# Kernel tuning notes

Measured on AMD Instinct MI355X. Metric: run time of the kernel, lower is better.

The kernel has to match this reference:

```python
import jax, jax.numpy as jnp
import numpy as np

B, G, N, D = 2, 2, 2048, 512
H, DH = 8, 64
DI = H * DH  # dim_inner = 512


def rmsnorm(x, gamma):
    # x: [b, g, n, d]; original normalizes over feature dim (F.normalize, eps=1e-12)
    norm = jnp.linalg.norm(x, axis=-1, keepdims=True)
    normed = x / jnp.maximum(norm, 1e-12)
    return normed * jnp.sqrt(jnp.asarray(x.shape[-1], x.dtype)) * gamma[None, :, None, :]


def setup_inputs() -> dict:
    key = jax.random.key(0)
    ks = jax.random.split(key, 8)
    x = jax.random.normal(ks[0], (B, G, N, D), dtype=jnp.float32)
    mask = jax.random.randint(ks[1], (B, N), 0, 2) > 0
    gamma_q = jnp.ones((G, D), dtype=jnp.float32)
    gamma_c = jnp.ones((G, D), dtype=jnp.float32)
    s = 0.02
    wq = jax.random.normal(ks[2], (G, DI, D), dtype=jnp.float32) * s
    wkv = jax.random.normal(ks[3], (G, 2 * DI, D), dtype=jnp.float32) * s
    wout = jax.random.normal(ks[4], (G, D, DI), dtype=jnp.float32) * s
    null_kv = jax.random.normal(ks[5], (2, G, H, 1, DH), dtype=jnp.float32)
    return {"x": x, "mask": mask, "gamma_q": gamma_q, "gamma_c": gamma_c,
            "wq": wq, "wkv": wkv, "wout": wout, "null_kv": null_kv}


def reference(x, mask, gamma_q, gamma_c, wq, wkv, wout, null_kv):
    b, g, n, d = x.shape
    # prenorm (context = x, so both norms applied to same input)
    xq = rmsnorm(x, gamma_q)
    xc = rmsnorm(x, gamma_c)
    # grouped 1x1 conv projections == per-group matmuls
    q = jnp.einsum('bgnd,ged->bgne', xq, wq)                 # [b,g,n,DI]
    kv = jnp.einsum('bgnd,ged->bgne', xc, wkv)               # [b,g,n,2*DI]
    k, v = jnp.split(kv, 2, axis=-1)
    def split_heads(t):
        return t.reshape(b, g, n, H, DH).transpose(0, 1, 3, 2, 4)  # [b,g,h,n,dh]
    q, k, v = map(split_heads, (q, k, v))
    # null kv: concat along sequence dim
    nk = jnp.broadcast_to(null_kv[0][None], (b, g, H, 1, DH))
    nv = jnp.broadcast_to(null_kv[1][None], (b, g, H, 1, DH))
    k = jnp.concatenate([nk, k], axis=-2)                    # [b,g,h,n+1,dh]
    v = jnp.concatenate([nv, v], axis=-2)
    # attention
    scale = DH ** -0.5
    scores = jnp.einsum('bghid,bghjd->bghij', q, k) * scale  # [b,g,h,n,n+1]
    m = jnp.concatenate([jnp.ones((b, 1), dtype=bool), mask], axis=-1)  # pad True for null kv
    scores = jnp.where(m[:, None, None, None, :], scores, jnp.asarray(-1e30, scores.dtype))
    attn = jax.nn.softmax(scores, axis=-1)
    out = jnp.einsum('bghij,bghjd->bghid', attn, v)          # [b,g,h,n,dh]
    out = out.transpose(0, 1, 3, 2, 4).reshape(b, g, n, DI)  # merge heads
    out = jnp.einsum('bgne,gde->bgnd', out, wout)
    return out
```

## Files before the change

### kernel.cpp

```cpp
#include <hip/hip_runtime.h>
#include <stdint.h>

typedef unsigned short u16;
typedef __attribute__((ext_vector_type(8))) short  bf16x8;
typedef __attribute__((ext_vector_type(8))) u16    u16x8;
typedef __attribute__((ext_vector_type(4))) u16    u16x4;
typedef __attribute__((ext_vector_type(4))) float  f32x4;
typedef __attribute__((ext_vector_type(2))) unsigned u32x2;

#define SEQ 2048
#define DIM 512
#define NH  8
#define NBG 4
#define QSCALE 0.18033688011112042f

__device__ __forceinline__ float bf2f(u16 u) { return __uint_as_float(((unsigned)u) << 16); }
__device__ __forceinline__ u16 f2bf(float f) {
  unsigned u = __float_as_uint(f);
  return (u16)((u + 0x7FFFu + ((u >> 16) & 1u)) >> 16);
}
__device__ __forceinline__ float h2f(u16 u) { return (float)__builtin_bit_cast(_Float16, u); }
__device__ __forceinline__ u16 f2h(float f) { return __builtin_bit_cast(unsigned short, (_Float16)f); }

__device__ __forceinline__ float ex2(float x) {
#if __has_builtin(__builtin_amdgcn_exp2f)
  return __builtin_amdgcn_exp2f(x);
#else
  return exp2f(x);
#endif
}

__device__ __forceinline__ void gload_lds16(const void* g, void* l) {
#if __has_builtin(__builtin_amdgcn_global_load_lds)
  __builtin_amdgcn_global_load_lds((__attribute__((address_space(1))) void*)g,
                                   (__attribute__((address_space(3))) void*)l, 16, 0, 0);
#else
  *(u16x8*)l = *(const u16x8*)g;
#endif
}

__device__ __forceinline__ int float_mode(const void* gq) {
  unsigned w0 = *(const unsigned*)gq;
  return (w0 == 0x3F800000u) ? 1 : ((w0 == 0x3C003C00u) ? 2 : 0);
}
__device__ __forceinline__ int mask_mode(const void* maskp) {
  const unsigned* mw = (const unsigned*)maskp;
  bool all01 = true, lowhit = false, f32ish = true;
#pragma unroll
  for (int i = 0; i < 64; i++) {
    unsigned v = mw[i];
    all01 = all01 && (v <= 1u);
    lowhit = lowhit || ((v & 0xFFFFu) == 0x3F80u) || ((v & 0xFFFFu) == 0x3C00u);
    f32ish = f32ish && (v == 0u || v == 0x3F800000u);
  }
  return all01 ? 0 : (lowhit ? 1 : (f32ish ? 2 : 3));
}
__device__ __forceinline__ bool mask_at(const void* m, int idx, int mode) {
  if (mode == 0) return ((const int*)m)[idx] != 0;
  if (mode == 1) return ((const u16*)m)[idx] != 0;
  if (mode == 2) return ((const float*)m)[idx] != 0.f;
  return ((const unsigned char*)m)[idx] != 0;
}
__device__ __forceinline__ float ldf(const void* p, int i, int mode) {
  if (mode == 1) return ((const float*)p)[i];
  if (mode == 2) return h2f(((const u16*)p)[i]);
  return bf2f(((const u16*)p)[i]);
}

__global__ __launch_bounds__(256) void pre_kernel(
    const void* __restrict__ x, const void* __restrict__ gq, const void* __restrict__ gc,
    const void* __restrict__ wq, const void* __restrict__ wkv, const void* __restrict__ wout,
    const void* __restrict__ nkv, const void* __restrict__ maskp,
    u16* __restrict__ wqb, u16* __restrict__ wkvb, u16* __restrict__ woutb, u16* __restrict__ nkvb,
    u16* __restrict__ xn, int* __restrict__ gidx, int* __restrict__ nv)
{
  const int NWQ = 2*512*512, NWKV = 2*1024*512, NWOUT = 2*512*512;
  if (blockIdx.x >= 3073) {
    __shared__ int sc[2][256];
    __shared__ int tot;
    int b = blockIdx.x - 3073;
    int t = threadIdx.x;
    const int smode = mask_mode(maskp);
    int base = t * 8;
    int loc[8]; int c = 0;
#pragma unroll
    for (int i = 0; i < 8; i++) { loc[i] = mask_at(maskp, b * SEQ + base + i, smode) ? 1 : 0; c += loc[i]; }
    sc[0][t] = c;
    int src = 0, v = c;
    for (int off = 1; off < 256; off <<= 1) {
      __syncthreads();
      int add = (t >= off) ? sc[src][t - off] : 0;
      v += add;
      sc[src ^ 1][t] = v;
      src ^= 1;
    }
    int run = v - c;
#pragma unroll
    for (int i = 0; i < 8; i++) { if (loc[i]) gidx[b * SEQ + run] = base + i; run += loc[i]; }
    if (t == 255) { nv[b] = v; tot = v; }
    __syncthreads();
#pragma unroll
    for (int i = 0; i < 8; i++) {
      int p = base + i;
      if (p >= tot) gidx[b * SEQ + p] = 0;
    }
    return;
  }
  int mode = float_mode(gq);
  if (blockIdx.x < 1025) {
    int loc = (blockIdx.x * 256 + threadIdx.x) * 8;
    const void* s; u16* d; int fold = 0; const void* gam = nullptr; int gbase = 0; float ex = 1.f;
    if (loc < NWQ) { s = wq; d = wqb; fold = 1; gam = gq; gbase = ((loc >> 18) << 9) | (loc & 511); ex = QSCALE; }
    else { loc -= NWQ;
      if (loc < NWKV) { s = wkv; d = wkvb; fold = 1; gam = gc; gbase = ((loc >> 19) << 9) | (loc & 511); }
      else { loc -= NWKV;
        if (loc < NWOUT) { s = wout; d = woutb; }
        else { loc -= NWOUT; if (loc < 2048) { s = nkv; d = nkvb; } else return; } } }
    u16x8 o;
#pragma unroll
    for (int j = 0; j < 8; j++) {
      float v = ldf(s, loc + j, mode) * ex;
      if (fold) v *= ldf(gam, gbase + j, mode);
      o[j] = f2bf(v);
    }
    *(u16x8*)(d + loc) = o;
    return;
  }
  int row  = (blockIdx.x - 1025) * 4 + (threadIdx.x >> 6);
  int lane = threadIdx.x & 63;
  float f[8];
  if (mode == 1) {
    const float* xr = (const float*)x + (size_t)row * DIM + lane * 8;
    f32x4 a = *(const f32x4*)xr, b2 = *(const f32x4*)(xr + 4);
#pragma unroll
    for (int i = 0; i < 4; i++) { f[i] = a[i]; f[i + 4] = b2[i]; }
  } else if (mode == 2) {
    u16x8 v = *(const u16x8*)((const u16*)x + (size_t)row * DIM + lane * 8);
#pragma unroll
    for (int i = 0; i < 8; i++) f[i] = h2f(v[i]);
  } else {
    u16x8 v = *(const u16x8*)((const u16*)x + (size_t)row * DIM + lane * 8);
#pragma unroll
    for (int i = 0; i < 8; i++) f[i] = bf2f(v[i]);
  }
  float ss = 0.f;
#pragma unroll
  for (int i = 0; i < 8; i++) ss += f[i] * f[i];
#pragma unroll
  for (int off = 32; off; off >>= 1) ss += __shfl_xor(ss, off);
  float scale = 22.62741699796952f / fmaxf(sqrtf(ss), 1e-12f);
  u16x8 o;
#pragma unroll
  for (int i = 0; i < 8; i++) o[i] = f2bf(f[i] * scale);
  *(u16x8*)(xn + (size_t)row * DIM + lane * 8) = o;
}

__global__ __launch_bounds__(256, 4) void gemm_qkv(
    const u16* __restrict__ A, const u16* __restrict__ wqb, const u16* __restrict__ wkvb,
    u16* __restrict__ qb, u16* __restrict__ kb, u16* __restrict__ vtb,
    const int* __restrict__ gidx, const int* __restrict__ nv)
{
  __shared__ u16 As[128 * 64], Bs[64 * 64];
  int bg = blockIdx.z, g = bg & 1;
  int y = blockIdx.y;
  const u16* Bw; int Ncols, bn0, isq;
  if (y < 8) { Bw = wqb;  Ncols = 512;  bn0 = y * 64;       isq = 1; }
  else       { Bw = wkvb; Ncols = 1024; bn0 = (y - 8) * 64; isq = 0; }
  const int M = SEQ, K = DIM, ldc = 512;
  int bm0 = blockIdx.x * 128;
  if (!isq) {
    int nvb = nv[bg >> 1];
    if (bm0 >= ((nvb + 127) & ~127)) return;
  }
  int tid = threadIdx.x, w = tid >> 6, l = tid & 63;
  int li = l & 15, lg = l >> 4;
  int wr = w >> 1, wc = w & 1;
  const u16* Ab = A + (size_t)bg * M * K;
  const u16* Bb = Bw + (size_t)g * Ncols * K;
  int arow[4];
#pragma unroll
  for (int i = 0; i < 4; i++) {
    int r = bm0 + ((i * 256 + tid) >> 3);
    arow[i] = isq ? r : gidx[(bg >> 1) * SEQ + r];
  }
  f32x4 acc[4][2];
#pragma unroll
  for (int m = 0; m < 4; m++)
#pragma unroll
    for (int n = 0; n < 2; n++) acc[m][n] = (f32x4){0.f, 0.f, 0.f, 0.f};
  for (int kt = 0; kt < K; kt += 64) {
#pragma unroll
    for (int i = 0; i < 4; i++) {
      int ch = i * 256 + tid;
      gload_lds16(Ab + (size_t)arow[i] * K + kt + ((ch & 7) << 3), &As[ch * 8]);
    }
#pragma unroll
    for (int i = 0; i < 2; i++) {
      int ch = i * 256 + tid;
      gload_lds16(Bb + (size_t)(bn0 + (ch >> 3)) * K + kt + ((ch & 7) << 3), &Bs[ch * 8]);
    }
    __syncthreads();
#pragma unroll
    for (int kk = 0; kk < 2; kk++) {
      bf16x8 a[4], b[2];
#pragma unroll
      for (int m = 0; m < 4; m++) a[m] = *(const bf16x8*)&As[(wr * 64 + m * 16 + li) * 64 + kk * 32 + lg * 8];
#pragma unroll
      for (int n = 0; n < 2; n++) b[n] = *(const bf16x8*)&Bs[(wc * 32 + n * 16 + li) * 64 + kk * 32 + lg * 8];
      __builtin_amdgcn_s_setprio(1);
#pragma unroll
      for (int m = 0; m < 4; m++)
#pragma unroll
        for (int n = 0; n < 2; n++)
          acc[m][n] = __builtin_amdgcn_mfma_f32_16x16x32_bf16(a[m], b[n], acc[m][n], 0, 0, 0);
      __builtin_amdgcn_s_setprio(0);
    }
    __syncthreads();
  }
  if (isq) {
#pragma unroll
    for (int m = 0; m < 4; m++) {
#pragma unroll
      for (int n = 0; n < 2; n++) {
        int row = bm0 + wr * 64 + m * 16 + lg * 4;
        int col = bn0 + wc * 32 + n * 16 + li;
        u16* cp = qb + (size_t)bg * M * ldc + (size_t)row * ldc + col;
#pragma unroll
        for (int r = 0; r < 4; r++) cp[(size_t)r * ldc] = f2bf(acc[m][n][r]);
      }
    }
  } else {
#pragma unroll
    for (int m = 0; m < 4; m++) {
#pragma unroll
      for (int n = 0; n < 2; n++) {
        int row = bm0 + wr * 64 + m * 16 + lg * 4;
        int col = bn0 + wc * 32 + n * 16 + li;
        if (col < 512) {
          u16* cp = kb + (size_t)bg * M * ldc + (size_t)row * ldc + col;
#pragma unroll
          for (int r = 0; r < 4; r++) cp[(size_t)r * ldc] = f2bf(acc[m][n][r]);
        } else {
          u16x4 pk;
#pragma unroll
          for (int r = 0; r < 4; r++) pk[r] = f2bf(acc[m][n][r]);
          *(u16x4*)&vtb[(size_t)bg * 512 * M + (size_t)(col - 512) * M + row] = pk;
        }
      }
    }
  }
}

__global__ __launch_bounds__(256, 4) void gemm_out(
    const u16* __restrict__ A, const u16* __restrict__ Bw,
    void* __restrict__ Cout, const void* __restrict__ gq0)
{
  __shared__ u16 As[128 * 64], Bs[64 * 64];
  const int M = SEQ, K = DIM, ldc = 512;
  int bg = blockIdx.z, g = bg & 1;
  int bm0 = blockIdx.x * 128, bn0 = blockIdx.y * 64;
  int tid = threadIdx.x, w = tid >> 6, l = tid & 63;
  int li = l & 15, lg = l >> 4;
  int wr = w >> 1, wc = w & 1;
  const u16* Ab = A + (size_t)bg * M * K;
  const u16* Bb = Bw + (size_t)g * 512 * K;
  f32x4 acc[4][2];
#pragma unroll
  for (int m = 0; m < 4; m++)
#pragma unroll
    for (int n = 0; n < 2; n++) acc[m][n] = (f32x4){0.f, 0.f, 0.f, 0.f};
  for (int kt = 0; kt < K; kt += 64) {
#pragma unroll
    for (int i = 0; i < 4; i++) {
      int ch = i * 256 + tid;
      gload_lds16(Ab + (size_t)(bm0 + (ch >> 3)) * K + kt + ((ch & 7) << 3), &As[ch * 8]);
    }
#pragma unroll
    for (int i = 0; i < 2; i++) {
      int ch = i * 256 + tid;
      gload_lds16(Bb + (size_t)(bn0 + (ch >> 3)) * K + kt + ((ch & 7) << 3), &Bs[ch * 8]);
    }
    __syncthreads();
#pragma unroll
    for (int kk = 0; kk < 2; kk++) {
      bf16x8 a[4], b[2];
#pragma unroll
      for (int m = 0; m < 4; m++) a[m] = *(const bf16x8*)&As[(wr * 64 + m * 16 + li) * 64 + kk * 32 + lg * 8];
#pragma unroll
      for (int n = 0; n < 2; n++) b[n] = *(const bf16x8*)&Bs[(wc * 32 + n * 16 + li) * 64 + kk * 32 + lg * 8];
      __builtin_amdgcn_s_setprio(1);
#pragma unroll
      for (int m = 0; m < 4; m++)
#pragma unroll
        for (int n = 0; n < 2; n++)
          acc[m][n] = __builtin_amdgcn_mfma_f32_16x16x32_bf16(a[m], b[n], acc[m][n], 0, 0, 0);
      __builtin_amdgcn_s_setprio(0);
    }
    __syncthreads();
  }
  int mode = float_mode(gq0);
#pragma unroll
  for (int m = 0; m < 4; m++) {
#pragma unroll
    for (int n = 0; n < 2; n++) {
      int row = bm0 + wr * 64 + m * 16 + lg * 4;
      int col = bn0 + wc * 32 + n * 16 + li;
      if (mode == 1) {
        float* cp = (float*)Cout + (size_t)bg * M * ldc + (size_t)row * ldc + col;
#pragma unroll
        for (int r = 0; r < 4; r++) cp[(size_t)r * ldc] = acc[m][n][r];
      } else if (mode == 2) {
        u16* cp = (u16*)Cout + (size_t)bg * M * ldc + (size_t)row * ldc + col;
#pragma unroll
        for (int r = 0; r < 4; r++) cp[(size_t)r * ldc] = f2h(acc[m][n][r]);
      } else {
        u16* cp = (u16*)Cout + (size_t)bg * M * ldc + (size_t)row * ldc + col;
#pragma unroll
        for (int r = 0; r < 4; r++) cp[(size_t)r * ldc] = f2bf(acc[m][n][r]);
      }
    }
  }
}

__global__ __launch_bounds__(256, 2) void attn_kernel(
    const u16* __restrict__ q, const u16* __restrict__ k, const u16* __restrict__ vt,
    const u16* __restrict__ nkv, const int* __restrict__ nv, u16* __restrict__ ao)
{
  __shared__ __align__(16) u16 Kb[2][64 * 64];
  __shared__ __align__(16) u16 Vb[2][64 * 64];
  __shared__ __align__(16) u16 Ps[4][16 * 72];
  const int bid = blockIdx.x;
  const int h = bid & 7, bg = (bid >> 3) & 3, ib = bid >> 5;
  const int g = bg & 1;
  const int tid = threadIdx.x, w = tid >> 6, l = tid & 63;
  const int li = l & 15, lg = l >> 4;
  const int i0 = ib * 128 + w * 32;
  const int nvb = nv[bg >> 1];
  const int NT = (nvb + 63) >> 6;

  auto stage = [&](int t, int buf) {
    int jb = t * 64;
#pragma unroll
    for (int p = 0; p < 2; p++) {
      int idx = p * 256 + tid;
      int r = idx >> 3, G = idx & 7;
      int c = (G ^ (r & 7)) << 3;
      gload_lds16(k + ((size_t)bg * SEQ + jb + r) * DIM + h * 64 + c, &Kb[buf][idx * 8]);
    }
#pragma unroll
    for (int p = 0; p < 2; p++) {
      int idx = p * 256 + tid;
      int r = idx >> 3, G = idx & 7;
      int c = (G ^ (r & 7)) << 3;
      gload_lds16(vt + ((size_t)bg * DIM + h * 64 + r) * SEQ + jb + c, &Vb[buf][idx * 8]);
    }
  };

  if (NT > 0) stage(0, 0);

  bf16x8 qf[2][2];
#pragma unroll
  for (int rg = 0; rg < 2; rg++)
#pragma unroll
    for (int kk = 0; kk < 2; kk++)
      qf[rg][kk] = *(const bf16x8*)&q[((size_t)bg * SEQ + i0 + rg * 16 + li) * DIM + h * 64 + kk * 32 + lg * 8];

  bf16x8 ones;
#pragma unroll
  for (int r = 0; r < 8; r++) ones[r] = (short)0x3F80;

  const u16* nk = nkv + ((size_t)g * NH + h) * 64;
  const u16* nvp = nkv + ((size_t)(2 + g) * NH + h) * 64;
  f32x4 oacc[2][4], lacc[2];
#pragma unroll
  for (int rg = 0; rg < 2; rg++) {
    float s = 0.f;
#pragma unroll
    for (int kk = 0; kk < 2; kk++)
#pragma unroll
      for (int r = 0; r < 8; r++)
        s += bf2f((u16)qf[rg][kk][r]) * bf2f(nk[kk * 32 + lg * 8 + r]);
    s += __shfl_xor(s, 16); s += __shfl_xor(s, 32);
    float pn = ex2(s);
    lacc[rg] = (f32x4){pn, pn, pn, pn};
#pragma unroll
    for (int dm = 0; dm < 4; dm++) {
      f32x4 o;
#pragma unroll
      for (int r = 0; r < 4; r++) o[r] = pn * bf2f(nvp[dm * 16 + lg * 4 + r]);
      oacc[rg][dm] = o;
    }
  }
  __syncthreads();

  for (int t = 0; t < NT; t++) {
    int cur = t & 1;
    if (t + 1 < NT) stage(t + 1, cur ^ 1);
    const bool tail = (t == NT - 1);

    bf16x8 kf[4][2];
#pragma unroll
    for (int jm = 0; jm < 4; jm++)
#pragma unroll
      for (int kk = 0; kk < 2; kk++) {
        int gsw = ((kk * 4 + lg) ^ (li & 7)) << 3;
        kf[jm][kk] = *(const bf16x8*)&Kb[cur][(jm * 16 + li) * 64 + gsw];
      }

    f32x4 s4[2][4];
    __builtin_amdgcn_s_setprio(1);
#pragma unroll
    for (int rg = 0; rg < 2; rg++)
#pragma unroll
      for (int jm = 0; jm < 4; jm++) {
        f32x4 z = {0.f, 0.f, 0.f, 0.f};
        z = __builtin_amdgcn_mfma_f32_16x16x32_bf16(kf[jm][0], qf[rg][0], z, 0, 0, 0);
        z = __builtin_amdgcn_mfma_f32_16x16x32_bf16(kf[jm][1], qf[rg][1], z, 0, 0, 0);
        s4[rg][jm] = z;
      }
    __builtin_amdgcn_s_setprio(0);

    int jb = t * 64;
#pragma unroll
    for (int rg = 0; rg < 2; rg++) {
      u16* pb = &Ps[w][0];
#pragma unroll
      for (int jm = 0; jm < 4; jm++) {
        unsigned u0 = __float_as_uint(ex2(s4[rg][jm][0]));
        unsigned u1 = __float_as_uint(ex2(s4[rg][jm][1]));
        unsigned u2 = __float_as_uint(ex2(s4[rg][jm][2]));
        unsigned u3 = __float_as_uint(ex2(s4[rg][jm][3]));
        unsigned w01 = __builtin_amdgcn_perm(u1, u0, 0x07060302u);
        unsigned w23 = __builtin_amdgcn_perm(u3, u2, 0x07060302u);
        if (tail) {
          int e0 = jb + jm * 16 + lg * 4;
          unsigned t01 = (e0 + 0 < nvb ? 0x0000FFFFu : 0u) | (e0 + 1 < nvb ? 0xFFFF0000u : 0u);
          unsigned t23 = (e0 + 2 < nvb ? 0x0000FFFFu : 0u) | (e0 + 3 < nvb ? 0xFFFF0000u : 0u);
          w01 &= t01; w23 &= t23;
        }
        *(u32x2*)&Ps[w][li * 72 + jm * 16 + lg * 4] = (u32x2){w01, w23};
      }
      bf16x8 pf0 = *(const bf16x8*)&pb[li * 72 + lg * 8];
      bf16x8 pf1 = *(const bf16x8*)&pb[li * 72 + 32 + lg * 8];
      __builtin_amdgcn_s_setprio(1);
      lacc[rg] = __builtin_amdgcn_mfma_f32_16x16x32_bf16(ones, pf0, lacc[rg], 0, 0, 0);
      lacc[rg] = __builtin_amdgcn_mfma_f32_16x16x32_bf16(ones, pf1, lacc[rg], 0, 0, 0);
#pragma unroll
      for (int dm = 0; dm < 4; dm++) {
        int gsw0 = ((0 * 4 + lg) ^ (li & 7)) << 3;
        int gsw1 = ((1 * 4 + lg) ^ (li & 7)) << 3;
        bf16x8 vf0 = *(const bf16x8*)&Vb[cur][(dm * 16 + li) * 64 + gsw0];
        bf16x8 vf1 = *(const bf16x8*)&Vb[cur][(dm * 16 + li) * 64 + gsw1];
        oacc[rg][dm] = __builtin_amdgcn_mfma_f32_16x16x32_bf16(vf0, pf0, oacc[rg][dm], 0, 0, 0);
        oacc[rg][dm] = __builtin_amdgcn_mfma_f32_16x16x32_bf16(vf1, pf1, oacc[rg][dm], 0, 0, 0);
      }
      __builtin_amdgcn_s_setprio(0);
    }
    __syncthreads();
  }

#pragma unroll
  for (int rg = 0; rg < 2; rg++) {
    float inv = 1.f / lacc[rg][0];
#pragma unroll
    for (int dm = 0; dm < 4; dm++) {
      u16x4 o;
#pragma unroll
      for (int r = 0; r < 4; r++) o[r] = f2bf(oacc[rg][dm][r] * inv);
      *(u16x4*)&ao[((size_t)bg * SEQ + i0 + rg * 16 + li) * DIM + h * 64 + dm * 16 + lg * 4] = o;
    }
  }
}

extern "C" void kernel_launch(void* const* d_in, const int* in_sizes, int n_in,
                              void* d_out, int out_size, void* d_ws, size_t ws_size,
                              hipStream_t stream) {
  const void* x    = d_in[0];
  const void* msk  = d_in[1];
  const void* gq   = d_in[2];
  const void* gc   = d_in[3];
  const void* wq   = d_in[4];
  const void* wkv  = d_in[5];
  const void* wout = d_in[6];
  const void* nkv  = d_in[7];

  u16* base = (u16*)d_ws;
  const size_t SLOT = (size_t)NBG * SEQ * DIM;
  u16* xn = base + 0 * SLOT;
  u16* ao = base + 0 * SLOT;
  u16* qb = base + 1 * SLOT;
  u16* kb = base + 2 * SLOT;
  u16* vt = base + 3 * SLOT;
  u16* wreg = base + 4 * SLOT;
  const int NWQ = 2 * 512 * 512, NWKV = 2 * 1024 * 512, NWOUT = 2 * 512 * 512;
  u16* wqb   = wreg;
  u16* wkvb  = wreg + NWQ;
  u16* woutb = wreg + NWQ + NWKV;
  u16* nkvb  = wreg + NWQ + NWKV + NWOUT;
  int* gidx  = (int*)(nkvb + 2048);
  int* nv    = gidx + 2 * SEQ;

  hipLaunchKernelGGL(pre_kernel, dim3(3075), dim3(256), 0, stream,
                     x, gq, gc, wq, wkv, wout, nkv, msk,
                     wqb, wkvb, woutb, nkvb, xn, gidx, nv);
  hipLaunchKernelGGL(gemm_qkv, dim3(16, 24, NBG), dim3(256), 0, stream,
                     xn, wqb, wkvb, qb, kb, vt, gidx, nv);
  hipLaunchKernelGGL(attn_kernel, dim3(512), dim3(256), 0, stream,
                     qb, kb, vt, nkvb, nv, ao);
  hipLaunchKernelGGL(gemm_out, dim3(16, 8, NBG), dim3(256), 0, stream,
                     ao, woutb, d_out, gq);
}
```

Before: 85.26 us.

## Use 32x32x16 MFMA in attention and feed P from registers via permuted V^T

The attention inner loop moves from 16x16x32 MFMAs to 32x32x16 MFMAs. The QK^T output register layout is now consumed directly as the B operand of the PV and row-sum MFMAs, which removes the per-wave LDS round trip through the Ps buffer. To make this work, the V^T store in the KV projection permutes rows within groups of 16 so that the key order matches the register layout of P. The risks are higher register pressure from the 16-wide accumulators and a required exact match between the permutation and the MFMA layout.

Result: no change. 84.71 us, median of 2 (-0.6%).

```diff
diff --git a/kernel.cpp b/kernel.cpp
--- a/kernel.cpp
+++ b/kernel.cpp
@@ -6,7 +6,9 @@
 typedef __attribute__((ext_vector_type(8))) u16    u16x8;
 typedef __attribute__((ext_vector_type(4))) u16    u16x4;
 typedef __attribute__((ext_vector_type(4))) float  f32x4;
+typedef __attribute__((ext_vector_type(16))) float f32x16;
 typedef __attribute__((ext_vector_type(2))) unsigned u32x2;
+typedef __attribute__((ext_vector_type(4))) unsigned u32x4;
 
 #define SEQ 2048
 #define DIM 512
@@ -244,7 +246,8 @@
           u16x4 pk;
 #pragma unroll
           for (int r = 0; r < 4; r++) pk[r] = f2bf(acc[m][n][r]);
-          *(u16x4*)&vtb[(size_t)bg * 512 * M + (size_t)(col - 512) * M + row] = pk;
+          int prow = (row & ~12) | ((row & 4) << 1) | ((row & 8) >> 1);
+          *(u16x4*)&vtb[(size_t)bg * 512 * M + (size_t)(col - 512) * M + prow] = pk;
         }
       }
     }
@@ -328,12 +331,12 @@
 {
   __shared__ __align__(16) u16 Kb[2][64 * 64];
   __shared__ __align__(16) u16 Vb[2][64 * 64];
-  __shared__ __align__(16) u16 Ps[4][16 * 72];
   const int bid = blockIdx.x;
   const int h = bid & 7, bg = (bid >> 3) & 3, ib = bid >> 5;
   const int g = bg & 1;
   const int tid = threadIdx.x, w = tid >> 6, l = tid & 63;
-  const int li = l & 15, lg = l >> 4;
+  const int lo = l & 31, hi = l >> 5;
+  const int dl7 = lo & 7;
   const int i0 = ib * 128 + w * 32;
   const int nvb = nv[bg >> 1];
   const int NT = (nvb + 63) >> 6;
@@ -358,12 +361,10 @@
 
   if (NT > 0) stage(0, 0);
 
-  bf16x8 qf[2][2];
-#pragma unroll
-  for (int rg = 0; rg < 2; rg++)
-#pragma unroll
-    for (int kk = 0; kk < 2; kk++)
-      qf[rg][kk] = *(const bf16x8*)&q[((size_t)bg * SEQ + i0 + rg * 16 + li) * DIM + h * 64 + kk * 32 + lg * 8];
+  bf16x8 qf[4];
+#pragma unroll
+  for (int ks = 0; ks < 4; ks++)
+    qf[ks] = *(const bf16x8*)&q[((size_t)bg * SEQ + i0 + lo) * DIM + h * 64 + ks * 16 + hi * 8];
 
   bf16x8 ones;
 #pragma unroll
@@ -371,25 +372,23 @@
 
   const u16* nk = nkv + ((size_t)g * NH + h) * 64;
   const u16* nvp = nkv + ((size_t)(2 + g) * NH + h) * 64;
-  f32x4 oacc[2][4], lacc[2];
-#pragma unroll
-  for (int rg = 0; rg < 2; rg++) {
-    float s = 0.f;
-#pragma unroll
-    for (int kk = 0; kk < 2; kk++)
-#pragma unroll
-      for (int r = 0; r < 8; r++)
-        s += bf2f((u16)qf[rg][kk][r]) * bf2f(nk[kk * 32 + lg * 8 + r]);
-    s += __shfl_xor(s, 16); s += __shfl_xor(s, 32);
-    float pn = ex2(s);
-    lacc[rg] = (f32x4){pn, pn, pn, pn};
-#pragma unroll
-    for (int dm = 0; dm < 4; dm++) {
-      f32x4 o;
-#pragma unroll
-      for (int r = 0; r < 4; r++) o[r] = pn * bf2f(nvp[dm * 16 + lg * 4 + r]);
-      oacc[rg][dm] = o;
-    }
+  f32x16 oacc[2], lacc;
+  {
+    float s0 = 0.f;
+#pragma unroll
+    for (int ks = 0; ks < 4; ks++)
+#pragma unroll
+      for (int e = 0; e < 8; e++)
+        s0 += bf2f((u16)qf[ks][e]) * bf2f(nk[ks * 16 + hi * 8 + e]);
+    s0 += __shfl_xor(s0, 32);
+    float pn = ex2(s0);
+#pragma unroll
+    for (int r = 0; r < 16; r++) lacc[r] = pn;
+#pragma unroll
+    for (int dblk = 0; dblk < 2; dblk++)
+#pragma unroll
+      for (int r = 0; r < 16; r++)
+        oacc[dblk][r] = pn * bf2f(nvp[dblk * 32 + (r & 3) + 8 * (r >> 2) + 4 * hi]);
   }
   __syncthreads();
 
@@ -397,79 +396,74 @@
     int cur = t & 1;
     if (t + 1 < NT) stage(t + 1, cur ^ 1);
     const bool tail = (t == NT - 1);
-
-    bf16x8 kf[4][2];
-#pragma unroll
-    for (int jm = 0; jm < 4; jm++)
-#pragma unroll
-      for (int kk = 0; kk < 2; kk++) {
-        int gsw = ((kk * 4 + lg) ^ (li & 7)) << 3;
-        kf[jm][kk] = *(const bf16x8*)&Kb[cur][(jm * 16 + li) * 64 + gsw];
-      }
-
-    f32x4 s4[2][4];
-    __builtin_amdgcn_s_setprio(1);
-#pragma unroll
-    for (int rg = 0; rg < 2; rg++)
-#pragma unroll
-      for (int jm = 0; jm < 4; jm++) {
-        f32x4 z = {0.f, 0.f, 0.f, 0.f};
-        z = __builtin_amdgcn_mfma_f32_16x16x32_bf16(kf[jm][0], qf[rg][0], z, 0, 0, 0);
-        z = __builtin_amdgcn_mfma_f32_16x16x32_bf16(kf[jm][1], qf[rg][1], z, 0, 0, 0);
-        s4[rg][jm] = z;
-      }
-    __builtin_amdgcn_s_setprio(0);
-
-    int jb = t * 64;
-#pragma unroll
-    for (int rg = 0; rg < 2; rg++) {
-      u16* pb = &Ps[w][0];
-#pragma unroll
-      for (int jm = 0; jm < 4; jm++) {
-        unsigned u0 = __float_as_uint(ex2(s4[rg][jm][0]));
-        unsigned u1 = __float_as_uint(ex2(s4[rg][jm][1]));
-        unsigned u2 = __float_as_uint(ex2(s4[rg][jm][2]));
-        unsigned u3 = __float_as_uint(ex2(s4[rg][jm][3]));
-        unsigned w01 = __builtin_amdgcn_perm(u1, u0, 0x07060302u);
-        unsigned w23 = __builtin_amdgcn_perm(u3, u2, 0x07060302u);
+    const u16* kb = &Kb[cur][0];
+    const u16* vb = &Vb[cur][0];
+
+    bf16x8 vf[2][4];
+#pragma unroll
+    for (int dblk = 0; dblk < 2; dblk++)
+#pragma unroll
+      for (int f = 0; f < 4; f++) {
+        int chunk = ((f * 2 + hi) ^ dl7) << 3;
+        vf[dblk][f] = *(const bf16x8*)&vb[(dblk * 32 + lo) * 64 + chunk];
+      }
+
+    unsigned U[2][4][2];
+#pragma unroll
+    for (int jblk = 0; jblk < 2; jblk++) {
+      f32x16 s;
+#pragma unroll
+      for (int r = 0; r < 16; r++) s[r] = 0.f;
+      __builtin_amdgcn_s_setprio(1);
+#pragma unroll
+      for (int ks = 0; ks < 4; ks++) {
+        bf16x8 kf = *(const bf16x8*)&kb[(jblk * 32 + lo) * 64 + (((ks * 2 + hi) ^ dl7) << 3)];
+        s = __builtin_amdgcn_mfma_f32_32x32x16_bf16(kf, qf[ks], s, 0, 0, 0);
+      }
+      __builtin_amdgcn_s_setprio(0);
+#pragma unroll
+      for (int a = 0; a < 4; a++) {
+        unsigned e0 = __float_as_uint(ex2(s[4 * a + 0]));
+        unsigned e1 = __float_as_uint(ex2(s[4 * a + 1]));
+        unsigned e2 = __float_as_uint(ex2(s[4 * a + 2]));
+        unsigned e3 = __float_as_uint(ex2(s[4 * a + 3]));
+        unsigned w01 = __builtin_amdgcn_perm(e1, e0, 0x07060302u);
+        unsigned w23 = __builtin_amdgcn_perm(e3, e2, 0x07060302u);
         if (tail) {
-          int e0 = jb + jm * 16 + lg * 4;
-          unsigned t01 = (e0 + 0 < nvb ? 0x0000FFFFu : 0u) | (e0 + 1 < nvb ? 0xFFFF0000u : 0u);
-          unsigned t23 = (e0 + 2 < nvb ? 0x0000FFFFu : 0u) | (e0 + 3 < nvb ? 0xFFFF0000u : 0u);
+          int j0 = t * 64 + jblk * 32 + 8 * a + 4 * hi;
+          unsigned t01 = (j0 + 0 < nvb ? 0x0000FFFFu : 0u) | (j0 + 1 < nvb ? 0xFFFF0000u : 0u);
+          unsigned t23 = (j0 + 2 < nvb ? 0x0000FFFFu : 0u) | (j0 + 3 < nvb ? 0xFFFF0000u : 0u);
           w01 &= t01; w23 &= t23;
         }
-        *(u32x2*)&Ps[w][li * 72 + jm * 16 + lg * 4] = (u32x2){w01, w23};
-      }
-      bf16x8 pf0 = *(const bf16x8*)&pb[li * 72 + lg * 8];
-      bf16x8 pf1 = *(const bf16x8*)&pb[li * 72 + 32 + lg * 8];
-      __builtin_amdgcn_s_setprio(1);
-      lacc[rg] = __builtin_amdgcn_mfma_f32_16x16x32_bf16(ones, pf0, lacc[rg], 0, 0, 0);
-      lacc[rg] = __builtin_amdgcn_mfma_f32_16x16x32_bf16(ones, pf1, lacc[rg], 0, 0, 0);
-#pragma unroll
-      for (int dm = 0; dm < 4; dm++) {
-        int gsw0 = ((0 * 4 + lg) ^ (li & 7)) << 3;
-        int gsw1 = ((1 * 4 + lg) ^ (li & 7)) << 3;
-        bf16x8 vf0 = *(const bf16x8*)&Vb[cur][(dm * 16 + li) * 64 + gsw0];
-        bf16x8 vf1 = *(const bf16x8*)&Vb[cur][(dm * 16 + li) * 64 + gsw1];
-        oacc[rg][dm] = __builtin_amdgcn_mfma_f32_16x16x32_bf16(vf0, pf0, oacc[rg][dm], 0, 0, 0);
-        oacc[rg][dm] = __builtin_amdgcn_mfma_f32_16x16x32_bf16(vf1, pf1, oacc[rg][dm], 0, 0, 0);
-      }
-      __builtin_amdgcn_s_setprio(0);
-    }
+        U[jblk][a][0] = w01;
+        U[jblk][a][1] = w23;
+      }
+    }
+    __builtin_amdgcn_s_setprio(1);
+#pragma unroll
+    for (int jblk = 0; jblk < 2; jblk++)
+#pragma unroll
+      for (int m = 0; m < 2; m++) {
+        bf16x8 pf = __builtin_bit_cast(bf16x8,
+          (u32x4){U[jblk][2 * m][0], U[jblk][2 * m][1], U[jblk][2 * m + 1][0], U[jblk][2 * m + 1][1]});
+        lacc    = __builtin_amdgcn_mfma_f32_32x32x16_bf16(ones, pf, lacc, 0, 0, 0);
+        oacc[0] = __builtin_amdgcn_mfma_f32_32x32x16_bf16(vf[0][jblk * 2 + m], pf, oacc[0], 0, 0, 0);
+        oacc[1] = __builtin_amdgcn_mfma_f32_32x32x16_bf16(vf[1][jblk * 2 + m], pf, oacc[1], 0, 0, 0);
+      }
+    __builtin_amdgcn_s_setprio(0);
     __syncthreads();
   }
 
-#pragma unroll
-  for (int rg = 0; rg < 2; rg++) {
-    float inv = 1.f / lacc[rg][0];
-#pragma unroll
-    for (int dm = 0; dm < 4; dm++) {
+  float inv = 1.f / lacc[0];
+#pragma unroll
+  for (int dblk = 0; dblk < 2; dblk++)
+#pragma unroll
+    for (int rq = 0; rq < 4; rq++) {
       u16x4 o;
 #pragma unroll
-      for (int r = 0; r < 4; r++) o[r] = f2bf(oacc[rg][dm][r] * inv);
-      *(u16x4*)&ao[((size_t)bg * SEQ + i0 + rg * 16 + li) * DIM + h * 64 + dm * 16 + lg * 4] = o;
-    }
-  }
+      for (int qq = 0; qq < 4; qq++) o[qq] = f2bf(oacc[dblk][4 * rq + qq] * inv);
+      *(u16x4*)&ao[((size_t)bg * SEQ + i0 + lo) * DIM + h * 64 + dblk * 32 + 8 * rq + 4 * hi] = o;
+    }
 }
 
 extern "C" void kernel_launch(void* const* d_in, const int* in_sizes, int n_in,
```
